# Kernel tuning notes

Hardware: AMD Instinct MI355X
Metric: run time of the kernel (lower is better)

## Reference

```python
import jax, jax.numpy as jnp
import numpy as np

B, N, DIM, HEAD = 4, 2048, 1024, 16
HD = DIM // HEAD
LN_EPS = 1e-5


def setup_inputs() -> dict:
    key = jax.random.key(0)
    k1, k2, k3, k4 = jax.random.split(key, 4)
    x = jax.random.normal(k1, (B, N, DIM), dtype=jnp.float32)
    A = jax.random.normal(k2, (B, N, HEAD, 1), dtype=jnp.float32)
    ln_w = jnp.ones((DIM,), dtype=jnp.float32)
    ln_b = jnp.zeros((DIM,), dtype=jnp.float32)
    Wqk = jax.random.normal(k3, (2 * DIM, DIM), dtype=jnp.float32) * (DIM ** -0.5)
    wv = jax.random.normal(k4, (1, 1), dtype=jnp.float32)
    return {"x": x, "A": A, "ln_w": ln_w, "ln_b": ln_b, "Wqk": Wqk, "wv": wv}


def reference(x, A, ln_w, ln_b, Wqk, wv):
    b, n, dim = x.shape
    head = A.shape[2]
    hd = dim // head
    scale = dim ** -0.5  # NOTE: source uses full-dim scale, not head_dim

    # LayerNorm
    mu = jnp.mean(x, axis=-1, keepdims=True)
    xc = x - mu
    var = jnp.mean(xc * xc, axis=-1, keepdims=True)
    xn = xc * jax.lax.rsqrt(var + LN_EPS) * ln_w + ln_b

    # QK projection: [B,N,2*dim] -> q,k [B,head,N,hd]
    qk = jnp.einsum('bnd,ed->bne', xn, Wqk)
    qk = qk.reshape(b, n, 2, head, hd)
    q = qk[:, :, 0].transpose(0, 2, 1, 3)  # [B,H,N,hd]
    k = qk[:, :, 1].transpose(0, 2, 1, 3)

    # v = Linear(1,1,bias=False)(A), head-major layout [B,H,N,1]
    v = (A * wv[0, 0]).transpose(0, 2, 1, 3)

    scores = jnp.einsum('bhnd,bhmd->bhnm', q, k) * scale  # [B,H,N,N]
    attn = jax.nn.softmax(scores, axis=-1)
    out = jnp.einsum('bhnm,bhme->bhne', attn, v)  # [B,H,N,1]
    A_plus = out.transpose(0, 2, 1, 3)  # [B,N,H,1]
    return A + A_plus
```

## Files before the change

kernel.cpp:

```cpp
#include <hip/hip_runtime.h>

#define B_    4
#define N_    2048
#define DIM_  1024
#define HEAD_ 16
#define HD_   64
#define M_    (B_*N_)
#define E_    (2*DIM_)

typedef short          frag8 __attribute__((ext_vector_type(8)));
typedef float          facc4 __attribute__((ext_vector_type(4)));
typedef unsigned short ush4  __attribute__((ext_vector_type(4)));
typedef _Float16       hv4   __attribute__((ext_vector_type(4)));
typedef _Float16       hv2   __attribute__((ext_vector_type(2)));

#define AS1 __attribute__((address_space(1)))
#define AS3 __attribute__((address_space(3)))

__device__ __forceinline__ void gld_lds16(const void* g, void* l) {
    __builtin_amdgcn_global_load_lds((AS1 void*)(void*)g, (AS3 void*)l, 16, 0, 0);
}

__device__ __forceinline__ unsigned short f2bf(float f) {
    return __builtin_bit_cast(unsigned short, (__bf16)f);
}

__global__ __launch_bounds__(256) void ln_kernel(const float* __restrict__ x,
                                                 const float* __restrict__ lw,
                                                 const float* __restrict__ lb,
                                                 unsigned short* __restrict__ xn) {
    const int row = blockIdx.x;
    const int t   = threadIdx.x;
    const float4 v = ((const float4*)(x + (size_t)row * DIM_))[t];
    float s  = v.x + v.y + v.z + v.w;
    float sq = v.x*v.x + v.y*v.y + v.z*v.z + v.w*v.w;
#pragma unroll
    for (int off = 32; off > 0; off >>= 1) {
        s  += __shfl_xor(s,  off);
        sq += __shfl_xor(sq, off);
    }
    __shared__ float red[8];
    const int w = t >> 6;
    if ((t & 63) == 0) { red[w] = s; red[4 + w] = sq; }
    __syncthreads();
    s  = red[0] + red[1] + red[2] + red[3];
    sq = red[4] + red[5] + red[6] + red[7];
    const float mu   = s * (1.0f / DIM_);
    const float rstd = rsqrtf(sq * (1.0f / DIM_) - mu * mu + 1e-5f);
    const float4 wv4 = ((const float4*)lw)[t];
    const float4 bv4 = ((const float4*)lb)[t];
    ush4 o;
    o[0] = f2bf((v.x - mu) * rstd * wv4.x + bv4.x);
    o[1] = f2bf((v.y - mu) * rstd * wv4.y + bv4.y);
    o[2] = f2bf((v.z - mu) * rstd * wv4.z + bv4.z);
    o[3] = f2bf((v.w - mu) * rstd * wv4.w + bv4.w);
    *(ush4*)(xn + (size_t)row * DIM_ + t * 4) = o;
}

__global__ __launch_bounds__(256) void cvt_kernel(const float* __restrict__ in,
                                                  unsigned short* __restrict__ outp) {
    const int i = blockIdx.x * 256 + threadIdx.x;
    const float4 v = ((const float4*)in)[i];
    ush4 o;
    o[0] = f2bf(v.x); o[1] = f2bf(v.y); o[2] = f2bf(v.z); o[3] = f2bf(v.w);
    ((ush4*)outp)[i] = o;
}

__global__ __launch_bounds__(256) void vprep_kernel(const float* __restrict__ A,
                                                    const float* __restrict__ wv,
                                                    unsigned short* __restrict__ v16) {
    const int bh = blockIdx.x;
    const int b = bh >> 4, h = bh & 15;
    const float wvv = wv[0];
#pragma unroll
    for (int i = 0; i < 8; ++i) {
        const int n = i * 256 + threadIdx.x;
        const float f = A[((size_t)(b * N_ + n)) * HEAD_ + h] * wvv;
        v16[(size_t)bh * N_ + n] = __builtin_bit_cast(unsigned short, (_Float16)f);
    }
}

__global__ __launch_bounds__(256) void gemm_qk(const unsigned short* __restrict__ xn,
                                               const unsigned short* __restrict__ wb,
                                               unsigned short* __restrict__ qo,
                                               unsigned short* __restrict__ ko) {
    __shared__ __attribute__((aligned(16))) unsigned short As[128 * 64];
    __shared__ __attribute__((aligned(16))) unsigned short Bs[128 * 64];
    const int t    = threadIdx.x;
    const int lane = t & 63;
    const int w    = t >> 6;
    const int wr   = w & 1, wc = w >> 1;
    const int lr   = lane & 15, lg = lane >> 4;
    const int bid  = blockIdx.x;
    const int xcd  = bid & 7;
    const int l    = bid >> 3;
    const int bm   = xcd * 8 + (l & 7);
    const int bn   = l >> 3;
    const int m0   = bm * 128, e0 = bn * 128;

    facc4 acc[4][4] = {};

    for (int k0 = 0; k0 < DIM_; k0 += 64) {
#pragma unroll
        for (int it = 0; it < 4; ++it) {
            const int seg = it * 256 + t;
            const int row = seg >> 3;
            const int ss  = (seg & 7) ^ (row & 7);
            unsigned short* dstA = (unsigned short*)As + (size_t)(it * 256 + (t & ~63)) * 8;
            unsigned short* dstB = (unsigned short*)Bs + (size_t)(it * 256 + (t & ~63)) * 8;
            gld_lds16(xn + (size_t)(m0 + row) * DIM_ + k0 + ss * 8, dstA);
            gld_lds16(wb + (size_t)(e0 + row) * DIM_ + k0 + ss * 8, dstB);
        }
        __syncthreads();

        frag8 af[4][2];
#pragma unroll
        for (int rt = 0; rt < 4; ++rt) {
            const int row = wr * 64 + rt * 16 + lr;
            const int sw  = (row & 7) << 4;
            af[rt][0] = *(const frag8*)((const char*)As + row * 128 + ((lg * 16) ^ sw));
            af[rt][1] = *(const frag8*)((const char*)As + row * 128 + ((64 + lg * 16) ^ sw));
        }
#pragma unroll
        for (int ct = 0; ct < 4; ++ct) {
            const int row = wc * 64 + ct * 16 + lr;
            const int sw  = (row & 7) << 4;
            const frag8 b0 = *(const frag8*)((const char*)Bs + row * 128 + ((lg * 16) ^ sw));
            const frag8 b1 = *(const frag8*)((const char*)Bs + row * 128 + ((64 + lg * 16) ^ sw));
#pragma unroll
            for (int rt = 0; rt < 4; ++rt) {
                acc[rt][ct] = __builtin_amdgcn_mfma_f32_16x16x32_bf16(af[rt][0], b0, acc[rt][ct], 0, 0, 0);
                acc[rt][ct] = __builtin_amdgcn_mfma_f32_16x16x32_bf16(af[rt][1], b1, acc[rt][ct], 0, 0, 0);
            }
        }
        __syncthreads();
    }

    const float QSCALE = 0.03125f * 1.4426950408889634f;
#pragma unroll
    for (int rt = 0; rt < 4; ++rt) {
#pragma unroll
        for (int ct = 0; ct < 4; ++ct) {
            const int eg = e0 + wc * 64 + ct * 16 + lr;
#pragma unroll
            for (int r = 0; r < 4; ++r) {
                const int   mg = m0 + wr * 64 + rt * 16 + lg * 4 + r;
                const int   b  = mg >> 11;
                const int   n  = mg & (N_ - 1);
                const float val = acc[rt][ct][r];
                if (eg < DIM_) {
                    const int h = eg >> 6, d = eg & 63;
                    qo[((size_t)((b * HEAD_ + h) * N_ + n)) * HD_ + d] = f2bf(val * QSCALE);
                } else {
                    const int e2 = eg - DIM_;
                    const int h = e2 >> 6, d = e2 & 63;
                    ko[((size_t)((b * HEAD_ + h) * N_ + n)) * HD_ + d] = f2bf(val);
                }
            }
        }
    }
}

__global__ __launch_bounds__(256) void attn_kernel(const unsigned short* __restrict__ q,
                                                   const unsigned short* __restrict__ kmat,
                                                   const unsigned short* __restrict__ v16,
                                                   float2* __restrict__ part) {
    __shared__ __attribute__((aligned(16))) char KsB[3 * 8192];
    const int t    = threadIdx.x;
    const int lane = t & 63, w = t >> 6;
    const int lr   = lane & 15, lg = lane >> 4;
    const int id    = blockIdx.x;
    const int split = id >> 9;
    const int bh    = (id >> 3) & 63;
    const int qblk  = id & 7;
    const int b     = bh >> 4, h = bh & 15;
    const int q0    = qblk * 256 + w * 64;

    const int row0  = t >> 3;
    const int koff  = row0 * HD_ + (((t & 7) ^ (row0 & 7)) * 8);
    const int wbase = (t & ~63) * 16;
    const int sw    = (lr & 7) << 4;
    const int off_h0 = lr * 128 + ((lg * 16) ^ sw);
    const int off_h1 = lr * 128 + ((64 + lg * 16) ^ sw);

    const unsigned short* qbase = q    + (size_t)bh * N_ * HD_;
    const unsigned short* kfix  = kmat + (size_t)bh * N_ * HD_ + (size_t)split * 512 * HD_;
    const unsigned short* vfix  = v16  + (size_t)bh * N_ + split * 512;

    frag8 qf[4][2];
#pragma unroll
    for (int qt = 0; qt < 4; ++qt) {
#pragma unroll
        for (int hh = 0; hh < 2; ++hh)
            qf[qt][hh] = *(const frag8*)(qbase + (size_t)(q0 + qt * 16 + lr) * HD_ + hh * 32 + lg * 8);
    }

    hv4 sel, one1;
#pragma unroll
    for (int j = 0; j < 4; ++j) {
        sel[j]  = (lr == 0) ? (_Float16)1.f : (_Float16)0.f;
        one1[j] = (lr == 1) ? (_Float16)1.f : (_Float16)0.f;
    }
    const facc4 z4 = {0.f, 0.f, 0.f, 0.f};
    facc4 acc[4] = {};

#define STAGE(c) do {                                                          \
        gld_lds16(kfix + (c) * 64 * HD_ + koff,                                \
                  KsB + ((c) % 3) * 8192 + wbase);                             \
        gld_lds16(kfix + (c) * 64 * HD_ + koff + 2048,                         \
                  KsB + ((c) % 3) * 8192 + 4096 + wbase);                      \
    } while (0)

#define CHUNK(c) do {                                                          \
        __builtin_amdgcn_s_setprio(1);                                         \
        _Pragma("unroll")                                                      \
        for (int ct = 0; ct < 4; ++ct) {                                       \
            const frag8 kf0 = *(const frag8*)(KsB + ((c) % 3) * 8192 + ct * 2048 + off_h0); \
            const frag8 kf1 = *(const frag8*)(KsB + ((c) % 3) * 8192 + ct * 2048 + off_h1); \
            const hv4 vv = *(const hv4*)(vfix + (c) * 64 + ct * 16 + lg * 4);  \
            const hv4 av = vv * sel + one1;                                    \
            _Pragma("unroll")                                                  \
            for (int qt = 0; qt < 4; ++qt) {                                   \
                facc4 s_ = __builtin_amdgcn_mfma_f32_16x16x32_bf16(kf0, qf[qt][0], z4, 0, 0, 0); \
                s_ = __builtin_amdgcn_mfma_f32_16x16x32_bf16(kf1, qf[qt][1], s_, 0, 0, 0); \
                const hv2 p01 = __builtin_bit_cast(hv2,                        \
                    __builtin_amdgcn_cvt_pkrtz(__builtin_amdgcn_exp2f(s_[0]),  \
                                               __builtin_amdgcn_exp2f(s_[1]))); \
                const hv2 p23 = __builtin_bit_cast(hv2,                        \
                    __builtin_amdgcn_cvt_pkrtz(__builtin_amdgcn_exp2f(s_[2]),  \
                                               __builtin_amdgcn_exp2f(s_[3]))); \
                hv4 pb; pb[0] = p01[0]; pb[1] = p01[1]; pb[2] = p23[0]; pb[3] = p23[1]; \
                acc[qt] = __builtin_amdgcn_mfma_f32_16x16x16f16(av, pb, acc[qt], 0, 0, 0); \
            }                                                                  \
        }                                                                      \
        __builtin_amdgcn_s_setprio(0);                                         \
    } while (0)

#define ITER_S(c, Nw) {                                                        \
        asm volatile("s_waitcnt vmcnt(" Nw ")" ::: "memory");                  \
        __builtin_amdgcn_s_barrier();                                          \
        asm volatile("" ::: "memory");                                         \
        STAGE((c) + 2);                                                        \
        CHUNK(c);                                                              \
    }
#define ITER_N(c, Nw) {                                                        \
        asm volatile("s_waitcnt vmcnt(" Nw ")" ::: "memory");                  \
        __builtin_amdgcn_s_barrier();                                          \
        asm volatile("" ::: "memory");                                         \
        CHUNK(c);                                                              \
    }

    STAGE(0);
    STAGE(1);
    ITER_S(0, "2") ITER_S(1, "2") ITER_S(2, "2") ITER_S(3, "2")
    ITER_S(4, "2") ITER_S(5, "2") ITER_N(6, "2") ITER_N(7, "0")

#undef STAGE
#undef CHUNK
#undef ITER_S
#undef ITER_N

    if (lg == 0) {
#pragma unroll
        for (int qt = 0; qt < 4; ++qt) {
            const int row = q0 + qt * 16 + lr;
            float2 pr; pr.x = acc[qt][0]; pr.y = acc[qt][1];
            part[(size_t)split * (M_ * HEAD_) + ((size_t)(b * N_ + row)) * HEAD_ + h] = pr;
        }
    }
}

__global__ __launch_bounds__(256) void reduce_kernel(const float2* __restrict__ part,
                                                     const float* __restrict__ Ain,
                                                     float* __restrict__ outp) {
    const int i = blockIdx.x * 256 + threadIdx.x;
    const float2 p0 = part[i];
    const float2 p1 = part[1 * (M_ * HEAD_) + i];
    const float2 p2 = part[2 * (M_ * HEAD_) + i];
    const float2 p3 = part[3 * (M_ * HEAD_) + i];
    outp[i] = Ain[i] + (p0.x + p1.x + p2.x + p3.x) / (p0.y + p1.y + p2.y + p3.y);
}

extern "C" void kernel_launch(void* const* d_in, const int* in_sizes, int n_in,
                              void* d_out, int out_size, void* d_ws, size_t ws_size,
                              hipStream_t stream) {
    const float* x   = (const float*)d_in[0];
    const float* A   = (const float*)d_in[1];
    const float* lw  = (const float*)d_in[2];
    const float* lb  = (const float*)d_in[3];
    const float* Wqk = (const float*)d_in[4];
    const float* wv  = (const float*)d_in[5];
    float* outp = (float*)d_out;

    char* ws = (char*)d_ws;
    unsigned short* xn  = (unsigned short*)(ws);
    unsigned short* wb  = (unsigned short*)(ws + 16u * 1024 * 1024);
    unsigned short* qb  = (unsigned short*)(ws + 20u * 1024 * 1024);
    unsigned short* kb  = (unsigned short*)(ws + 36u * 1024 * 1024);
    unsigned short* v16 = (unsigned short*)(ws + 52u * 1024 * 1024);
    float2*         part = (float2*)(ws);

    ln_kernel<<<M_, 256, 0, stream>>>(x, lw, lb, xn);
    cvt_kernel<<<(E_ * DIM_ / 4) / 256, 256, 0, stream>>>(Wqk, wb);
    vprep_kernel<<<B_ * HEAD_, 256, 0, stream>>>(A, wv, v16);
    gemm_qk<<<64 * 16, 256, 0, stream>>>(xn, wb, qb, kb);
    attn_kernel<<<2048, 256, 0, stream>>>(qb, kb, v16, part);
    reduce_kernel<<<(M_ * HEAD_) / 256, 256, 0, stream>>>(part, A, outp);
}
```

Before: 117.2 us.

## Merge prep kernels and rewrite QK GEMM as 256x256 double-buffered pipeline

The LayerNorm, weight-cast and V-prep kernels become one launch that picks its work by block index, which removes two launches. The QK projection GEMM moves from 128x128 tiles with 256 threads to 256x256 tiles with 512 threads, on a one-wave grid of 256 blocks. K-tiles are double-buffered in 128KB of LDS. Global-to-LDS loads are interleaved across four MFMA sub-phases, using explicit vmcnt waits and raised wave priority, so memory traffic overlaps compute. The large LDS footprint allows only one block per CU, and the hand-ordered wait counts are fragile.

```diff
diff --git a/kernel.cpp b/kernel.cpp
--- a/kernel.cpp
+++ b/kernel.cpp
@@ -25,136 +25,202 @@
     return __builtin_bit_cast(unsigned short, (__bf16)f);
 }
 
-__global__ __launch_bounds__(256) void ln_kernel(const float* __restrict__ x,
-                                                 const float* __restrict__ lw,
-                                                 const float* __restrict__ lb,
-                                                 unsigned short* __restrict__ xn) {
-    const int row = blockIdx.x;
+__global__ __launch_bounds__(256) void prep_kernel(const float* __restrict__ x,
+                                                   const float* __restrict__ lw,
+                                                   const float* __restrict__ lb,
+                                                   const float* __restrict__ Wqk,
+                                                   const float* __restrict__ A,
+                                                   const float* __restrict__ wv,
+                                                   unsigned short* __restrict__ xn,
+                                                   unsigned short* __restrict__ wb,
+                                                   unsigned short* __restrict__ v16) {
+    __shared__ float red[8];
+    const int bid = blockIdx.x;
     const int t   = threadIdx.x;
-    const float4 v = ((const float4*)(x + (size_t)row * DIM_))[t];
-    float s  = v.x + v.y + v.z + v.w;
-    float sq = v.x*v.x + v.y*v.y + v.z*v.z + v.w*v.w;
-#pragma unroll
-    for (int off = 32; off > 0; off >>= 1) {
-        s  += __shfl_xor(s,  off);
-        sq += __shfl_xor(sq, off);
-    }
-    __shared__ float red[8];
-    const int w = t >> 6;
-    if ((t & 63) == 0) { red[w] = s; red[4 + w] = sq; }
-    __syncthreads();
-    s  = red[0] + red[1] + red[2] + red[3];
-    sq = red[4] + red[5] + red[6] + red[7];
-    const float mu   = s * (1.0f / DIM_);
-    const float rstd = rsqrtf(sq * (1.0f / DIM_) - mu * mu + 1e-5f);
-    const float4 wv4 = ((const float4*)lw)[t];
-    const float4 bv4 = ((const float4*)lb)[t];
-    ush4 o;
-    o[0] = f2bf((v.x - mu) * rstd * wv4.x + bv4.x);
-    o[1] = f2bf((v.y - mu) * rstd * wv4.y + bv4.y);
-    o[2] = f2bf((v.z - mu) * rstd * wv4.z + bv4.z);
-    o[3] = f2bf((v.w - mu) * rstd * wv4.w + bv4.w);
-    *(ush4*)(xn + (size_t)row * DIM_ + t * 4) = o;
-}
-
-__global__ __launch_bounds__(256) void cvt_kernel(const float* __restrict__ in,
-                                                  unsigned short* __restrict__ outp) {
-    const int i = blockIdx.x * 256 + threadIdx.x;
-    const float4 v = ((const float4*)in)[i];
-    ush4 o;
-    o[0] = f2bf(v.x); o[1] = f2bf(v.y); o[2] = f2bf(v.z); o[3] = f2bf(v.w);
-    ((ush4*)outp)[i] = o;
-}
-
-__global__ __launch_bounds__(256) void vprep_kernel(const float* __restrict__ A,
-                                                    const float* __restrict__ wv,
-                                                    unsigned short* __restrict__ v16) {
-    const int bh = blockIdx.x;
-    const int b = bh >> 4, h = bh & 15;
-    const float wvv = wv[0];
-#pragma unroll
-    for (int i = 0; i < 8; ++i) {
-        const int n = i * 256 + threadIdx.x;
-        const float f = A[((size_t)(b * N_ + n)) * HEAD_ + h] * wvv;
-        v16[(size_t)bh * N_ + n] = __builtin_bit_cast(unsigned short, (_Float16)f);
-    }
-}
-
-__global__ __launch_bounds__(256) void gemm_qk(const unsigned short* __restrict__ xn,
-                                               const unsigned short* __restrict__ wb,
-                                               unsigned short* __restrict__ qo,
-                                               unsigned short* __restrict__ ko) {
-    __shared__ __attribute__((aligned(16))) unsigned short As[128 * 64];
-    __shared__ __attribute__((aligned(16))) unsigned short Bs[128 * 64];
+    if (bid < M_) {
+        const float4 v = ((const float4*)(x + (size_t)bid * DIM_))[t];
+        float s  = v.x + v.y + v.z + v.w;
+        float sq = v.x*v.x + v.y*v.y + v.z*v.z + v.w*v.w;
+#pragma unroll
+        for (int off = 32; off > 0; off >>= 1) {
+            s  += __shfl_xor(s,  off);
+            sq += __shfl_xor(sq, off);
+        }
+        const int w = t >> 6;
+        if ((t & 63) == 0) { red[w] = s; red[4 + w] = sq; }
+        __syncthreads();
+        s  = red[0] + red[1] + red[2] + red[3];
+        sq = red[4] + red[5] + red[6] + red[7];
+        const float mu   = s * (1.0f / DIM_);
+        const float rstd = rsqrtf(sq * (1.0f / DIM_) - mu * mu + 1e-5f);
+        const float4 wv4 = ((const float4*)lw)[t];
+        const float4 bv4 = ((const float4*)lb)[t];
+        ush4 o;
+        o[0] = f2bf((v.x - mu) * rstd * wv4.x + bv4.x);
+        o[1] = f2bf((v.y - mu) * rstd * wv4.y + bv4.y);
+        o[2] = f2bf((v.z - mu) * rstd * wv4.z + bv4.z);
+        o[3] = f2bf((v.w - mu) * rstd * wv4.w + bv4.w);
+        *(ush4*)(xn + (size_t)bid * DIM_ + t * 4) = o;
+    } else if (bid < M_ + 2048) {
+        const int i = (bid - M_) * 256 + t;
+        const float4 v = ((const float4*)Wqk)[i];
+        ush4 o;
+        o[0] = f2bf(v.x); o[1] = f2bf(v.y); o[2] = f2bf(v.z); o[3] = f2bf(v.w);
+        ((ush4*)wb)[i] = o;
+    } else {
+        const int bh = bid - (M_ + 2048);
+        const int b = bh >> 4, h = bh & 15;
+        const float wvv = wv[0];
+#pragma unroll
+        for (int i = 0; i < 8; ++i) {
+            const int n = i * 256 + t;
+            const float f = A[((size_t)(b * N_ + n)) * HEAD_ + h] * wvv;
+            v16[(size_t)bh * N_ + n] = __builtin_bit_cast(unsigned short, (_Float16)f);
+        }
+    }
+}
+
+__global__ __launch_bounds__(512, 2) void gemm_qk(const unsigned short* __restrict__ xn,
+                                                  const unsigned short* __restrict__ wb,
+                                                  unsigned short* __restrict__ qo,
+                                                  unsigned short* __restrict__ ko) {
+    __shared__ __attribute__((aligned(16))) char lds[131072];
     const int t    = threadIdx.x;
     const int lane = t & 63;
-    const int w    = t >> 6;
-    const int wr   = w & 1, wc = w >> 1;
+    const int wid  = t >> 6;
+    const int wr   = wid >> 2, wc = wid & 3;
     const int lr   = lane & 15, lg = lane >> 4;
     const int bid  = blockIdx.x;
-    const int xcd  = bid & 7;
-    const int l    = bid >> 3;
-    const int bm   = xcd * 8 + (l & 7);
-    const int bn   = l >> 3;
-    const int m0   = bm * 128, e0 = bn * 128;
-
-    facc4 acc[4][4] = {};
-
-    for (int k0 = 0; k0 < DIM_; k0 += 64) {
-#pragma unroll
-        for (int it = 0; it < 4; ++it) {
-            const int seg = it * 256 + t;
-            const int row = seg >> 3;
-            const int ss  = (seg & 7) ^ (row & 7);
-            unsigned short* dstA = (unsigned short*)As + (size_t)(it * 256 + (t & ~63)) * 8;
-            unsigned short* dstB = (unsigned short*)Bs + (size_t)(it * 256 + (t & ~63)) * 8;
-            gld_lds16(xn + (size_t)(m0 + row) * DIM_ + k0 + ss * 8, dstA);
-            gld_lds16(wb + (size_t)(e0 + row) * DIM_ + k0 + ss * 8, dstB);
-        }
-        __syncthreads();
-
-        frag8 af[4][2];
-#pragma unroll
-        for (int rt = 0; rt < 4; ++rt) {
-            const int row = wr * 64 + rt * 16 + lr;
-            const int sw  = (row & 7) << 4;
-            af[rt][0] = *(const frag8*)((const char*)As + row * 128 + ((lg * 16) ^ sw));
-            af[rt][1] = *(const frag8*)((const char*)As + row * 128 + ((64 + lg * 16) ^ sw));
-        }
-#pragma unroll
-        for (int ct = 0; ct < 4; ++ct) {
-            const int row = wc * 64 + ct * 16 + lr;
-            const int sw  = (row & 7) << 4;
-            const frag8 b0 = *(const frag8*)((const char*)Bs + row * 128 + ((lg * 16) ^ sw));
-            const frag8 b1 = *(const frag8*)((const char*)Bs + row * 128 + ((64 + lg * 16) ^ sw));
-#pragma unroll
-            for (int rt = 0; rt < 4; ++rt) {
-                acc[rt][ct] = __builtin_amdgcn_mfma_f32_16x16x32_bf16(af[rt][0], b0, acc[rt][ct], 0, 0, 0);
-                acc[rt][ct] = __builtin_amdgcn_mfma_f32_16x16x32_bf16(af[rt][1], b1, acc[rt][ct], 0, 0, 0);
-            }
-        }
-        __syncthreads();
-    }
+    const int bm   = bid & 31, bn = bid >> 5;
+    const int m0   = bm * 256, e0 = bn * 256;
+
+    const int srow = t >> 3;
+    const int ss8  = ((t & 7) ^ (srow & 7)) * 8;
+    const int wu16 = (t & ~63) * 16;
+
+    facc4 acc[8][4] = {};
+    frag8 a[4][2], b[2][2];
+
+#define STG(mat, tile, half) do {                                              \
+        const unsigned short* sp_ = (mat) ? wb : xn;                           \
+        const int rb_ = (mat) ? e0 : m0;                                       \
+        _Pragma("unroll")                                                      \
+        for (int l_ = 0; l_ < 2; ++l_)                                         \
+            gld_lds16(sp_ + (size_t)(rb_ + (half)*128 + l_*64 + srow) * DIM_   \
+                          + (tile)*64 + ss8,                                   \
+                      lds + ((tile)&1)*65536 + (mat)*32768 + (half)*16384      \
+                          + l_*8192 + wu16);                                   \
+    } while (0)
+
+#define LDA(mh) do {                                                           \
+        _Pragma("unroll")                                                      \
+        for (int mf_ = 0; mf_ < 4; ++mf_) {                                    \
+            const int row_ = wr*128 + (mh)*64 + mf_*16 + lr;                   \
+            const int sw_  = (row_ & 7) << 4;                                  \
+            const char* ab_ = lds + cb*65536;                                  \
+            a[mf_][0] = *(const frag8*)(ab_ + row_*128 + ((lg*16) ^ sw_));     \
+            a[mf_][1] = *(const frag8*)(ab_ + row_*128 + ((64 + lg*16) ^ sw_));\
+        }                                                                      \
+    } while (0)
+
+#define LDB(nh) do {                                                           \
+        _Pragma("unroll")                                                      \
+        for (int nf_ = 0; nf_ < 2; ++nf_) {                                    \
+            const int row_ = wc*64 + (nh)*32 + nf_*16 + lr;                    \
+            const int sw_  = (row_ & 7) << 4;                                  \
+            const char* bb_ = lds + cb*65536 + 32768;                          \
+            b[nf_][0] = *(const frag8*)(bb_ + row_*128 + ((lg*16) ^ sw_));     \
+            b[nf_][1] = *(const frag8*)(bb_ + row_*128 + ((64 + lg*16) ^ sw_));\
+        }                                                                      \
+    } while (0)
+
+#define MM(mh, nh) do {                                                        \
+        __builtin_amdgcn_s_setprio(1);                                         \
+        _Pragma("unroll")                                                      \
+        for (int mf_ = 0; mf_ < 4; ++mf_)                                      \
+        _Pragma("unroll")                                                      \
+        for (int nf_ = 0; nf_ < 2; ++nf_) {                                    \
+            acc[(mh)*4+mf_][(nh)*2+nf_] = __builtin_amdgcn_mfma_f32_16x16x32_bf16( \
+                a[mf_][0], b[nf_][0], acc[(mh)*4+mf_][(nh)*2+nf_], 0, 0, 0);   \
+            acc[(mh)*4+mf_][(nh)*2+nf_] = __builtin_amdgcn_mfma_f32_16x16x32_bf16( \
+                a[mf_][1], b[nf_][1], acc[(mh)*4+mf_][(nh)*2+nf_], 0, 0, 0);   \
+        }                                                                      \
+        __builtin_amdgcn_s_setprio(0);                                         \
+    } while (0)
+
+#define PH_SYNC(NW) do {                                                       \
+        asm volatile("s_waitcnt vmcnt(" NW ")" ::: "memory");                  \
+        __builtin_amdgcn_s_barrier();                                          \
+        asm volatile("" ::: "memory");                                         \
+    } while (0)
+#define PH_BAR() do {                                                          \
+        __builtin_amdgcn_s_barrier();                                          \
+        asm volatile("" ::: "memory");                                         \
+    } while (0)
+#define PH_LGKM() do {                                                         \
+        asm volatile("s_waitcnt lgkmcnt(0)" ::: "memory");                     \
+        __builtin_amdgcn_sched_barrier(0);                                     \
+    } while (0)
+
+    STG(0, 0, 0);  STG(1, 0, 0);  STG(0, 0, 1);  STG(1, 0, 1);
+    STG(0, 1, 0);  STG(0, 1, 1);  STG(1, 1, 0);
+
+    for (int m = 0; m < 15; ++m) {
+        const int cb = m & 1;
+        PH_SYNC("8");
+        LDA(0); LDB(0);
+        STG(1, m + 1, 1);
+        PH_LGKM();
+        MM(0, 0);
+        PH_SYNC("8");
+        LDB(1);
+        if (m <= 13) STG(0, m + 2, 0);
+        PH_LGKM();
+        MM(0, 1);
+        PH_SYNC("8");
+        LDA(1); LDB(0);
+        PH_LGKM();
+        MM(1, 0);
+        PH_SYNC("8");
+        LDB(1);
+        if (m <= 13) { STG(0, m + 2, 1); STG(1, m + 2, 0); }
+        PH_LGKM();
+        MM(1, 1);
+    }
+    {
+        const int cb = 1;
+        PH_SYNC("2");  LDA(0); LDB(0); PH_LGKM(); MM(0, 0);
+        PH_SYNC("0");  LDB(1);         PH_LGKM(); MM(0, 1);
+        PH_BAR();      LDA(1); LDB(0); PH_LGKM(); MM(1, 0);
+        PH_BAR();      LDB(1);         PH_LGKM(); MM(1, 1);
+    }
+#undef STG
+#undef LDA
+#undef LDB
+#undef MM
+#undef PH_SYNC
+#undef PH_BAR
+#undef PH_LGKM
 
     const float QSCALE = 0.03125f * 1.4426950408889634f;
 #pragma unroll
-    for (int rt = 0; rt < 4; ++rt) {
-#pragma unroll
-        for (int ct = 0; ct < 4; ++ct) {
-            const int eg = e0 + wc * 64 + ct * 16 + lr;
+    for (int mf8 = 0; mf8 < 8; ++mf8) {
+#pragma unroll
+        for (int nf4 = 0; nf4 < 4; ++nf4) {
+            const int eg = e0 + wc * 64 + nf4 * 16 + lr;
 #pragma unroll
             for (int r = 0; r < 4; ++r) {
-                const int   mg = m0 + wr * 64 + rt * 16 + lg * 4 + r;
-                const int   b  = mg >> 11;
+                const int   mg = m0 + wr * 128 + mf8 * 16 + lg * 4 + r;
+                const int   b_  = mg >> 11;
                 const int   n  = mg & (N_ - 1);
-                const float val = acc[rt][ct][r];
+                const float val = acc[mf8][nf4][r];
                 if (eg < DIM_) {
                     const int h = eg >> 6, d = eg & 63;
-                    qo[((size_t)((b * HEAD_ + h) * N_ + n)) * HD_ + d] = f2bf(val * QSCALE);
+                    qo[((size_t)((b_ * HEAD_ + h) * N_ + n)) * HD_ + d] = f2bf(val * QSCALE);
                 } else {
                     const int e2 = eg - DIM_;
                     const int h = e2 >> 6, d = e2 & 63;
-                    ko[((size_t)((b * HEAD_ + h) * N_ + n)) * HD_ + d] = f2bf(val);
+                    ko[((size_t)((b_ * HEAD_ + h) * N_ + n)) * HD_ + d] = f2bf(val);
                 }
             }
         }
@@ -300,10 +366,8 @@
     unsigned short* v16 = (unsigned short*)(ws + 52u * 1024 * 1024);
     float2*         part = (float2*)(ws);
 
-    ln_kernel<<<M_, 256, 0, stream>>>(x, lw, lb, xn);
-    cvt_kernel<<<(E_ * DIM_ / 4) / 256, 256, 0, stream>>>(Wqk, wb);
-    vprep_kernel<<<B_ * HEAD_, 256, 0, stream>>>(A, wv, v16);
-    gemm_qk<<<64 * 16, 256, 0, stream>>>(xn, wb, qb, kb);
+    prep_kernel<<<M_ + 2048 + B_ * HEAD_, 256, 0, stream>>>(x, lw, lb, Wqk, A, wv, xn, wb, v16);
+    gemm_qk<<<256, 512, 0, stream>>>(xn, wb, qb, kb);
     attn_kernel<<<2048, 256, 0, stream>>>(qb, kb, v16, part);
     reduce_kernel<<<(M_ * HEAD_) / 256, 256, 0, stream>>>(part, A, outp);
 }
```

After: 103.0 us. 1.14x faster.
